# Kernel tuning notes

Hardware: AMD Instinct MI355X
Metric: run time of the kernel (lower is better)

## Reference

```python
import jax, jax.numpy as jnp
import numpy as np

B, S, D = 2, 512, 256      # batch, seq_len, d_model
N = 16                     # d_state
DC = 4                     # d_conv
DI = 2 * D                 # d_inner
CHUNK = 32                 # scan remat chunk size (S % CHUNK == 0)


def setup_inputs() -> dict:
    key = jax.random.key(0)
    ks = jax.random.split(key, 10)
    sc = 0.02
    return {
        "x": jax.random.normal(ks[0], (B, S, D), jnp.float32),
        "adjacency_matrix": jax.random.uniform(ks[1], (B, S, S), dtype=jnp.float32),
        "ln_w": jnp.ones((D,), jnp.float32),
        "ln_b": jnp.zeros((D,), jnp.float32),
        "W_in": jax.random.normal(ks[2], (2 * DI, D), jnp.float32) * sc,
        "conv_w": jax.random.normal(ks[3], (DI, DI, DC), jnp.float32) * sc,
        "conv_b": jnp.zeros((DI,), jnp.float32),
        "W_xp": jax.random.normal(ks[4], (2 * N + 1, DI), jnp.float32) * sc,
        "W_dt": jax.random.normal(ks[5], (DI, 1), jnp.float32) * sc,
        "b_dt": jnp.zeros((DI,), jnp.float32),
        "Wr": jax.random.normal(ks[6], (N, N), jnp.float32) * sc,
        "br": jnp.zeros((N,), jnp.float32),
        "W_out": jax.random.normal(ks[7], (D, DI), jnp.float32) * sc,
    }


def _forward(x, adj, ln_w, ln_b, W_in, conv_w, conv_b, W_xp, W_dt, b_dt, Wr, br, W_out):
    residual = x
    # LayerNorm (biased variance, eps=1e-5, matching nn.LayerNorm)
    mu = x.mean(-1, keepdims=True)
    var = ((x - mu) ** 2).mean(-1, keepdims=True)
    xn = (x - mu) * jax.lax.rsqrt(var + 1e-5) * ln_w + ln_b
    # in_proj (no bias), chunk into x branch and gate z
    xz = xn @ W_in.T                                  # [B,S,2*DI]
    xp, z = xz[..., :DI], xz[..., DI:]
    # causal-ish conv1d with padding d_conv-1, then slice to seq_len
    xc = jax.lax.conv_general_dilated(
        xp.transpose(0, 2, 1), conv_w, (1,), [(DC - 1, DC - 1)],
        dimension_numbers=("NCH", "OIH", "NCH"))
    xc = (xc + conv_b[None, :, None])[..., :S].transpose(0, 2, 1)  # [B,S,DI]
    x_act = jax.nn.silu(xc)
    # x_proj (no bias) -> delta(1), B(N), C(N)
    ssm = x_act @ W_xp.T                              # [B,S,2N+1]
    delta = jax.nn.softplus(ssm[..., :1] @ W_dt.T + b_dt)  # [B,S,DI]
    Bm, Cm = ssm[..., 1:1 + N], ssm[..., 1 + N:]      # [B,S,N]
    pos = jnp.arange(S)

    def step(carry, xs):
        h, hist = xs_carry = carry
        t, d_t, B_t, C_t, x_t, a_t = xs
        # exponential-decay state update: h [B,DI,N]
        h = h * jnp.exp(-d_t)[..., None] + x_t[..., None] * B_t[:, None, :]
        # adjacency-gated, degree-normalized aggregation over prior states
        w = a_t * (pos < t)                           # [B,S], zeros for s>=t
        deg = jnp.maximum(w.sum(-1), 1.0)             # clamp(min=1.0)
        g = jnp.einsum('bs,sbdn->bdn', w, hist) / deg[:, None, None]
        boost = 0.1 * jax.nn.silu(g @ Wr.T + br)
        # torch skips the boost when t==0 or all causal weights are zero
        h = h + jnp.where((t > 0) & jnp.any(w > 0), boost, jnp.zeros_like(boost))
        hist = hist.at[t].set(h)
        y = jnp.einsum('bdn,bn->bd', h, C_t)
        return (h, hist), y

    xs = (pos,
          delta.transpose(1, 0, 2), Bm.transpose(1, 0, 2), Cm.transpose(1, 0, 2),
          x_act.transpose(1, 0, 2), adj.transpose(1, 0, 2))
    nchunks = S // CHUNK
    xs = jax.tree_util.tree_map(lambda a: a.reshape(nchunks, CHUNK, *a.shape[1:]), xs)
    carry0 = (jnp.zeros((B, DI, N), jnp.float32),
              jnp.zeros((S, B, DI, N), jnp.float32))

    @jax.checkpoint
    def chunk_body(carry, xs_c):
        return jax.lax.scan(step, carry, xs_c)

    _, ys = jax.lax.scan(chunk_body, carry0, xs)
    y = ys.reshape(S, B, DI).transpose(1, 0, 2)       # [B,S,DI]
    return (y * jax.nn.silu(z)) @ W_out.T + residual


def reference(x, adjacency_matrix, ln_w, ln_b, W_in, conv_w, conv_b, W_xp, W_dt, b_dt, Wr, br, W_out):
    return _forward(x, adjacency_matrix, ln_w, ln_b, W_in, conv_w, conv_b,
                    W_xp, W_dt, b_dt, Wr, br, W_out)
```

## Files before the change

### kernel.cpp

```cpp
#include <hip/hip_runtime.h>
#include <math.h>

static constexpr int B  = 2;
static constexpr int S  = 512;
static constexpr int D  = 256;
static constexpr int N  = 16;
static constexpr int DI = 512;
static constexpr int CHUNK = 32;
static constexpr int NCHUNK = S / CHUNK;
static constexpr int NL2 = 4;
static constexpr int DN = DI * N;
static constexpr int NSLOT = 8;

typedef unsigned int uint32;
typedef unsigned short ushort16;
using bf16x8 = __attribute__((ext_vector_type(8))) short;
using f32x4  = __attribute__((ext_vector_type(4))) float;

__device__ __forceinline__ ushort16 f2bf(float f) {
    uint32 u = __float_as_uint(f);
    u = (u + 0x7fffu + ((u >> 16) & 1u)) >> 16;
    return (ushort16)u;
}
__device__ __forceinline__ float bflo(uint32 u) { return __uint_as_float(u << 16); }
__device__ __forceinline__ float bfhi(uint32 u) { return __uint_as_float(u & 0xffff0000u); }
__device__ __forceinline__ float bf2f(ushort16 u) { return __uint_as_float(((uint32)u) << 16); }
__device__ __forceinline__ uint32 pk2(float a, float b) {
    return (uint32)(ushort16)f2bf(a) | ((uint32)(ushort16)f2bf(b) << 16);
}
template<int K>
__device__ __forceinline__ float rork(float x) {
    return __uint_as_float((uint32)__builtin_amdgcn_mov_dpp(
        (int)__float_as_uint(x), 0x120 + K, 0xf, 0xf, false));
}
__device__ __forceinline__ size_t htIdx(int b, int dn, int sb) {
    return ((size_t)(b * (S / 32) + sb) * DN + dn) * 32;
}

__global__ void ln_k(const float* __restrict__ x, const float* __restrict__ w,
                     const float* __restrict__ bias, ushort16* __restrict__ xnb) {
    int row = blockIdx.x;
    int lane = threadIdx.x;
    float4 v = *(const float4*)(x + row * D + lane * 4);
    float s = v.x + v.y + v.z + v.w;
    float q = v.x * v.x + v.y * v.y + v.z * v.z + v.w * v.w;
    for (int m = 1; m < 64; m <<= 1) { s += __shfl_xor(s, m); q += __shfl_xor(q, m); }
    float mu  = s * (1.0f / D);
    float var = q * (1.0f / D) - mu * mu;
    float rs  = rsqrtf(var + 1e-5f);
    float4 wv = *(const float4*)(w + lane * 4);
    float4 bv = *(const float4*)(bias + lane * 4);
    float4 o;
    o.x = (v.x - mu) * rs * wv.x + bv.x;
    o.y = (v.y - mu) * rs * wv.y + bv.y;
    o.z = (v.z - mu) * rs * wv.z + bv.z;
    o.w = (v.w - mu) * rs * wv.w + bv.w;
    uint2 pk;
    pk.x = pk2(o.x, o.y);
    pk.y = pk2(o.z, o.w);
    *(uint2*)(xnb + row * D + lane * 4) = pk;
}

template<int MODE>
__global__ __launch_bounds__(256) void gemmb_k(const ushort16* __restrict__ A,
                                               const float* __restrict__ W,
                                               const float* __restrict__ res,
                                               float* __restrict__ C,
                                               ushort16* __restrict__ xpb,
                                               float* __restrict__ zs,
                                               int M, int Nc, int K) {
    __shared__ __align__(16) short As[64 * 40];
    __shared__ __align__(16) short Ws[64 * 40];
    int tid = threadIdx.x;
    int l = tid & 63, wid = tid >> 6;
    int wm = wid & 1, wn = wid >> 1;
    int row0 = blockIdx.y * 64, col0 = blockIdx.x * 64;
    int r = tid >> 2, kseg = (tid & 3) * 8;
    f32x4 acc[2][2] = {};
    for (int k0 = 0; k0 < K; k0 += 32) {
        *(uint4*)&As[r * 40 + kseg] = *(const uint4*)(A + (size_t)(row0 + r) * K + k0 + kseg);
        {
            const float* wrow = W + (size_t)(col0 + r) * K + k0 + kseg;
            float4 w0 = *(const float4*)wrow;
            float4 w1 = *(const float4*)(wrow + 4);
            uint4 q;
            q.x = pk2(w0.x, w0.y); q.y = pk2(w0.z, w0.w);
            q.z = pk2(w1.x, w1.y); q.w = pk2(w1.z, w1.w);
            *(uint4*)&Ws[r * 40 + kseg] = q;
        }
        __syncthreads();
        bf16x8 aF[2], bF[2];
        #pragma unroll
        for (int am = 0; am < 2; ++am)
            aF[am] = *(const bf16x8*)&As[(wm * 32 + am * 16 + (l & 15)) * 40 + (l >> 4) * 8];
        #pragma unroll
        for (int bn = 0; bn < 2; ++bn)
            bF[bn] = *(const bf16x8*)&Ws[(wn * 32 + bn * 16 + (l & 15)) * 40 + (l >> 4) * 8];
        #pragma unroll
        for (int am = 0; am < 2; ++am)
            #pragma unroll
            for (int bn = 0; bn < 2; ++bn)
                acc[am][bn] = __builtin_amdgcn_mfma_f32_16x16x32_bf16(aF[am], bF[bn], acc[am][bn], 0, 0, 0);
        __syncthreads();
    }
    #pragma unroll
    for (int am = 0; am < 2; ++am)
        #pragma unroll
        for (int bn = 0; bn < 2; ++bn) {
            int cc = col0 + wn * 32 + bn * 16 + (l & 15);
            #pragma unroll
            for (int reg = 0; reg < 4; ++reg) {
                int rr = row0 + wm * 32 + am * 16 + (l >> 4) * 4 + reg;
                float v = acc[am][bn][reg];
                if (MODE == 0) {
                    if (res) v += res[(size_t)rr * Nc + cc];
                    C[(size_t)rr * Nc + cc] = v;
                } else {
                    int b = rr >> 9, t = rr & (S - 1);
                    if (cc < DI)
                        xpb[((size_t)(b * (S + 3) + 3 + t)) * DI + cc] = f2bf(v);
                    else
                        zs[((size_t)(b * S + t)) * DI + (cc - DI)] = v / (1.0f + __expf(-v));
                }
            }
        }
}

__global__ __launch_bounds__(256) void convm_k(const ushort16* __restrict__ xpb,
                                               const float* __restrict__ conv_w,
                                               const float* __restrict__ conv_b,
                                               float* __restrict__ x_act) {
    __shared__ __align__(16) short AxS[35 * 40];
    __shared__ __align__(16) short WbS[4 * 32 * 40];
    int tid = threadIdx.x;
    int l = tid & 63, wid = tid >> 6;
    int wm = wid & 1, wn = wid >> 1;
    int o0 = blockIdx.x * 32;
    int mt = blockIdx.y;
    int b = mt >> 4, tl0 = (mt & 15) * 32;
    f32x4 acc = {0.f, 0.f, 0.f, 0.f};

    for (int k0 = 0; k0 < DI; k0 += 32) {
        if (tid < 140) {
            int rr = tid >> 2, seg = tid & 3;
            uint4 v = *(const uint4*)(xpb + ((size_t)(b * (S + 3) + tl0 + rr)) * DI + k0 + seg * 8);
            *(uint4*)&AxS[rr * 40 + seg * 8] = v;
        }
        #pragma unroll
        for (int it = 0; it < 4; ++it) {
            int p = it * 256 + tid;
            int o = p >> 5, i = p & 31;
            float4 w4 = *(const float4*)(conv_w + ((size_t)(o0 + o) * DI + (k0 + i)) * 4);
            WbS[(0 * 32 + o) * 40 + i] = (short)f2bf(w4.x);
            WbS[(1 * 32 + o) * 40 + i] = (short)f2bf(w4.y);
            WbS[(2 * 32 + o) * 40 + i] = (short)f2bf(w4.z);
            WbS[(3 * 32 + o) * 40 + i] = (short)f2bf(w4.w);
        }
        __syncthreads();
        #pragma unroll
        for (int k = 0; k < 4; ++k) {
            bf16x8 aF = *(const bf16x8*)&AxS[(wm * 16 + (l & 15) + k) * 40 + (l >> 4) * 8];
            bf16x8 bF = *(const bf16x8*)&WbS[(k * 32 + wn * 16 + (l & 15)) * 40 + (l >> 4) * 8];
            acc = __builtin_amdgcn_mfma_f32_16x16x32_bf16(aF, bF, acc, 0, 0, 0);
        }
        __syncthreads();
    }
    int oc = o0 + wn * 16 + (l & 15);
    float bia = conv_b[oc];
    #pragma unroll
    for (int reg = 0; reg < 4; ++reg) {
        int m = wm * 16 + (l >> 4) * 4 + reg;
        float v = acc[reg] + bia;
        x_act[((size_t)(b * S + tl0 + m)) * DI + oc] = v / (1.0f + __expf(-v));
    }
}

__global__ void ssmE_k(const float* __restrict__ x_act, const float* __restrict__ W_xp,
                       const float* __restrict__ W_dt, const float* __restrict__ b_dt,
                       float* __restrict__ Bm, float* __restrict__ Cm,
                       float* __restrict__ E) {
    int row = blockIdx.x * 4 + (threadIdx.x >> 6);
    int lane = threadIdx.x & 63;
    const float* xr = x_act + (size_t)row * DI + lane * 8;
    float4 v0 = *(const float4*)xr;
    float4 v1 = *(const float4*)(xr + 4);
    float dtr = 0.0f;
    for (int j = 0; j < 2 * N + 1; ++j) {
        const float* wr = W_xp + (size_t)j * DI + lane * 8;
        float4 w0 = *(const float4*)wr;
        float4 w1 = *(const float4*)(wr + 4);
        float acc = v0.x * w0.x + v0.y * w0.y + v0.z * w0.z + v0.w * w0.w
                  + v1.x * w1.x + v1.y * w1.y + v1.z * w1.z + v1.w * w1.w;
        for (int m = 1; m < 64; m <<= 1) acc += __shfl_xor(acc, m);
        if (j == 0) dtr = acc;
        if (lane == 0) {
            if (j >= 1 && j < 1 + N) Bm[(size_t)row * N + (j - 1)] = acc;
            else if (j >= 1 + N)     Cm[(size_t)row * N + (j - 1 - N)] = acc;
        }
    }
    int d0 = lane * 8;
    float4 w0 = *(const float4*)(W_dt + d0);
    float4 w1 = *(const float4*)(W_dt + d0 + 4);
    float4 q0 = *(const float4*)(b_dt + d0);
    float4 q1 = *(const float4*)(b_dt + d0 + 4);
    float4 e0, e1;
    e0.x = 1.0f / (1.0f + __expf(dtr * w0.x + q0.x));
    e0.y = 1.0f / (1.0f + __expf(dtr * w0.y + q0.y));
    e0.z = 1.0f / (1.0f + __expf(dtr * w0.z + q0.z));
    e0.w = 1.0f / (1.0f + __expf(dtr * w0.w + q0.w));
    e1.x = 1.0f / (1.0f + __expf(dtr * w1.x + q1.x));
    e1.y = 1.0f / (1.0f + __expf(dtr * w1.y + q1.y));
    e1.z = 1.0f / (1.0f + __expf(dtr * w1.z + q1.z));
    e1.w = 1.0f / (1.0f + __expf(dtr * w1.w + q1.w));
    *(float4*)(E + (size_t)row * DI + d0) = e0;
    *(float4*)(E + (size_t)row * DI + d0 + 4) = e1;
}

__global__ void deg_k(const float* __restrict__ adj, float* __restrict__ rdeg, int* __restrict__ flagI) {
    int t = blockIdx.x & (S - 1), b = blockIdx.x >> 9;
    int lane = threadIdx.x;
    const float* row = adj + ((size_t)(b * S + t)) * S;
    float s = 0.0f; bool anyp = false;
    for (int i = lane; i < t; i += 64) { float v = row[i]; s += v; anyp |= (v > 0.0f); }
    for (int m = 1; m < 64; m <<= 1) s += __shfl_xor(s, m);
    bool any = __any(anyp);
    if (lane == 0) {
        rdeg[b * S + t] = 1.0f / fmaxf(s, 1.0f);
        if (t > 0 && any) atomicOr(flagI + t, 1);
    }
}

#define SCAN32(RO, ADJT, GSUM)                                              \
    _Pragma("unroll")                                                       \
    for (int j = 0; j < CHUNK; ++j) {                                       \
        float e  = eL [((RO) + j) * 8 + grp];                               \
        float xa = xaL[((RO) + j) * 8 + grp];                               \
        float Bn = BnL[((RO) + j) * 16 + n];                                \
        h = h * e + xa * Bn;                                                \
        float g0 = GSUM[j], g1 = 0.f, g2 = 0.f, g3 = 0.f;                   \
        const float* ar = (ADJT) + j * 36;                                  \
        int sp = 0;                                                         \
        _Pragma("unroll")                                                   \
        for (; sp + 4 <= j; sp += 4) {                                      \
            float4 av = *(const float4*)(ar + sp);                          \
            g0 += av.x * hreg[sp];     g1 += av.y * hreg[sp + 1];           \
            g2 += av.z * hreg[sp + 2]; g3 += av.w * hreg[sp + 3];           \
        }                                                                   \
        _Pragma("unroll")                                                   \
        for (; sp < j; ++sp) g0 += ar[sp] * hreg[sp];                       \
        float gr = (g0 + g1) + (g2 + g3);                                   \
        float m0 = gr * wrr[0] + rork<4>(gr) * wrr[4]                       \
                 + rork<8>(gr) * wrr[8] + rork<12>(gr) * wrr[12];           \
        float m1 = rork<1>(gr) * wrr[1] + rork<5>(gr) * wrr[5]              \
                 + rork<9>(gr) * wrr[9] + rork<13>(gr) * wrr[13];           \
        float m2 = rork<2>(gr) * wrr[2] + rork<6>(gr) * wrr[6]              \
                 + rork<10>(gr) * wrr[10] + rork<14>(gr) * wrr[14];         \
        float m3 = rork<3>(gr) * wrr[3] + rork<7>(gr) * wrr[7]              \
                 + rork<11>(gr) * wrr[11] + rork<15>(gr) * wrr[15];         \
        float acc = fmaf(rdegL[(RO) + j], (m0 + m1) + (m2 + m3), brn);      \
        if (flL[(RO) + j])                                                  \
            h = fmaf(0.1f * acc,                                            \
                     __builtin_amdgcn_rcpf(1.0f + __expf(-acc)), h);        \
        hreg[j] = h;                                                        \
    }

#define PRESUM(GSUM, PTR) {                                                 \
    const ushort16* _p = (PTR);                                             \
    _Pragma("unroll")                                                       \
    for (int qi = 0; qi < 4; ++qi) {                                        \
        uint4 q = *(const uint4*)(_p + qi * 8);                             \
        GSUM[qi*8+0] += bflo(q.x); GSUM[qi*8+1] += bfhi(q.x);               \
        GSUM[qi*8+2] += bflo(q.y); GSUM[qi*8+3] += bfhi(q.y);               \
        GSUM[qi*8+4] += bflo(q.z); GSUM[qi*8+5] += bfhi(q.z);               \
        GSUM[qi*8+6] += bflo(q.w); GSUM[qi*8+7] += bfhi(q.w);               \
    } }

#define HWRITE(CIDX, HTBUF) {                                               \
    ushort16* ht = histT + htIdx(b, dn, (CIDX));                            \
    _Pragma("unroll")                                                       \
    for (int qi = 0; qi < 4; ++qi) {                                        \
        uint4 q;                                                            \
        q.x = pk2(hreg[qi*8+0], hreg[qi*8+1]);                              \
        q.y = pk2(hreg[qi*8+2], hreg[qi*8+3]);                              \
        q.z = pk2(hreg[qi*8+4], hreg[qi*8+5]);                              \
        q.w = pk2(hreg[qi*8+6], hreg[qi*8+7]);                              \
        *(uint4*)(ht + qi * 8) = q;                                         \
        *(uint4*)&(HTBUF)[qi * 1024 + tid * 8] = q;                         \
    } }

#define MIDPHASE(TCL) {                                                     \
    int w = tid >> 6, l = tid & 63;                                         \
    int ksg = (l >> 4) * 8;                                                 \
    f32x4 ac0[4] = {}, ac1[4] = {};                                         \
    _Pragma("unroll")                                                       \
    for (int sidx = 0; sidx < (TCL); ++sidx) {                              \
        const float* p0 = adj + ((size_t)(b * S + c0s + (TCL) * 32 + (l & 15))) * S \
                        + c0s + sidx * 32 + ksg;                            \
        const float* p1 = p0 + 16 * S;                                      \
        float4 a00 = *(const float4*)p0, a01 = *(const float4*)(p0 + 4);    \
        float4 a10 = *(const float4*)p1, a11 = *(const float4*)(p1 + 4);    \
        uint4 qa, qb;                                                       \
        qa.x = pk2(a00.x, a00.y); qa.y = pk2(a00.z, a00.w);                 \
        qa.z = pk2(a01.x, a01.y); qa.w = pk2(a01.z, a01.w);                 \
        qb.x = pk2(a10.x, a10.y); qb.y = pk2(a10.z, a10.w);                 \
        qb.z = pk2(a11.x, a11.y); qb.w = pk2(a11.z, a11.w);                 \
        bf16x8 aF0, aF1;                                                    \
        *(uint4*)&aF0 = qa; *(uint4*)&aF1 = qb;                             \
        const short* hTs = hTarr[sidx];                                     \
        _Pragma("unroll")                                                   \
        for (int dblk = 0; dblk < 4; ++dblk) {                              \
            int col = w * 64 + dblk * 16 + (l & 15);                        \
            bf16x8 bF = *(const bf16x8*)&hTs[(l >> 4) * 1024 + col * 8];    \
            ac0[dblk] = __builtin_amdgcn_mfma_f32_16x16x32_bf16(aF0, bF, ac0[dblk], 0, 0, 0); \
            ac1[dblk] = __builtin_amdgcn_mfma_f32_16x16x32_bf16(aF1, bF, ac1[dblk], 0, 0, 0); \
        }                                                                   \
    }                                                                       \
    int jb0 = (l >> 4) * 4;                                                 \
    _Pragma("unroll")                                                       \
    for (int dblk = 0; dblk < 4; ++dblk) {                                  \
        int col = w * 64 + dblk * 16 + (l & 15);                            \
        _Pragma("unroll")                                                   \
        for (int reg = 0; reg < 4; ++reg) {                                 \
            Gmid[(jb0 + reg) * 136 + col]      = (short)f2bf(ac0[dblk][reg]); \
            Gmid[(16 + jb0 + reg) * 136 + col] = (short)f2bf(ac1[dblk][reg]); \
        }                                                                   \
    } }

#define GSADD(GSUM)                                                         \
    _Pragma("unroll")                                                       \
    for (int j = 0; j < CHUNK; ++j)                                         \
        GSUM[j] += bf2f((ushort16)Gmid[j * 136 + tid]);

__global__ __launch_bounds__(256) void chunk4_k(const float* __restrict__ adj,
                                                const float* __restrict__ x_act,
                                                const float* __restrict__ E,
                                                const float* __restrict__ Bm,
                                                const float* __restrict__ rdeg,
                                                const int* __restrict__ flagI,
                                                const float* __restrict__ Wr,
                                                const float* __restrict__ br,
                                                ushort16* __restrict__ Gall,
                                                ushort16* __restrict__ histT,
                                                float* __restrict__ hlast, int lc) {
    __shared__ __align__(16) char smem[51200];
    int tid = threadIdx.x;
    int c0 = 4 * lc;
    int c0s = c0 * CHUNK;
    const size_t SLOT = (size_t)B * DN * 32;
    int rp = lc & 1, wp = (lc + 1) & 1;

    if (blockIdx.x < 128) {
        float* triA  = (float*)smem;
        float* triB  = (float*)(smem + 4608);
        float* eL    = (float*)(smem + 9216);
        float* xaL   = (float*)(smem + 11264);
        float* BnL   = (float*)(smem + 13312);
        float* rdegL = (float*)(smem + 17408);
        int*   flL   = (int*)  (smem + 17664);
        short* hTA   = (short*)(smem + 17920);
        short* hTB   = (short*)(smem + 26112);
        short* hTC   = (short*)(smem + 34304);
        short* Gmid  = (short*)(smem + 42496);
        short* hTD   = (short*)(smem + 42496);

        int b = blockIdx.x >> 6;
        int d0 = (blockIdx.x & 63) << 3;
        int n = tid & 15, grp = (tid >> 4) & 7;
        int d = d0 + grp;
        int dn = d * N + n;
        int dnbase = (blockIdx.x & 63) << 7;
        const short* hTarr[4] = {hTA, hTB, hTC, hTD};

        {
            int j = tid >> 3, s4 = (tid & 7) * 4;
            {
                float4 a0 = *(const float4*)(adj + ((size_t)(b * S + c0s + j)) * S + c0s + s4);
                float* dp = triA + j * 36 + s4;
                dp[0] = a0.x; dp[1] = a0.y; dp[2] = a0.z; dp[3] = a0.w;
            }
            {
                float4 a0 = *(const float4*)(adj + ((size_t)(b * S + c0s + 32 + j)) * S + c0s + 32 + s4);
                float* dp = triB + j * 36 + s4;
                dp[0] = a0.x; dp[1] = a0.y; dp[2] = a0.z; dp[3] = a0.w;
            }
            int jr = tid >> 2, dd = (tid & 3) * 2;
            float2 ev = *(const float2*)(E     + ((size_t)(b * S + c0s + jr)) * DI + d0 + dd);
            float2 xv = *(const float2*)(x_act + ((size_t)(b * S + c0s + jr)) * DI + d0 + dd);
            eL [jr * 8 + dd] = ev.x; eL [jr * 8 + dd + 1] = ev.y;
            xaL[jr * 8 + dd] = xv.x; xaL[jr * 8 + dd + 1] = xv.y;
            int nn = (tid & 3) * 4;
            float4 bv = *(const float4*)(Bm + ((size_t)(b * S + c0s + jr)) * N + nn);
            BnL[jr * 16 + nn] = bv.x; BnL[jr * 16 + nn + 1] = bv.y;
            BnL[jr * 16 + nn + 2] = bv.z; BnL[jr * 16 + nn + 3] = bv.w;
            if (tid < 64) {
                rdegL[tid] = rdeg[b * S + c0s + tid];
                flL[tid]   = flagI[c0s + tid];
            }
        }
        __syncthreads();

        float gs0[CHUNK], gs1[CHUNK];
        float wrr[16];
        float brn = 0.f, h = 0.f;
        float hreg[CHUNK];

        if (tid < 128) {
            #pragma unroll
            for (int j = 0; j < CHUNK; ++j) { gs0[j] = 0.f; gs1[j] = 0.f; }
            size_t tb = ((size_t)b * DN + dn) * 32;
            if (lc >= 2) {
                PRESUM(gs0, Gall + ((size_t)rp * NSLOT + 0) * SLOT + tb);
                PRESUM(gs1, Gall + ((size_t)rp * NSLOT + 1) * SLOT + tb);
            }
            if (lc >= 1) {
                PRESUM(gs0, Gall + ((size_t)rp * NSLOT + 4) * SLOT + tb);
                PRESUM(gs1, Gall + ((size_t)rp * NSLOT + 5) * SLOT + tb);
            }
            int probe = __builtin_amdgcn_mov_dpp((int)n, 0x121, 0xf, 0xf, false);
            bool plusdir = (probe == ((n + 1) & 15));
            #pragma unroll
            for (int k = 0; k < 16; ++k) {
                int ip = (n + k) & 15, im = (n - k + 16) & 15;
                wrr[k] = Wr[n * 16 + (plusdir ? ip : im)];
            }
            brn = br[n];
            h = (lc == 0) ? 0.0f : hlast[b * DN + dn];

            SCAN32(0, triA, gs0)
            HWRITE(c0 + 0, hTA)
        }
        __syncthreads();
        if (tid < 128) MIDPHASE(1)
        __syncthreads();
        if (tid < 128) {
            GSADD(gs1)
            SCAN32(32, triB, gs1)
            HWRITE(c0 + 1, hTB)
        }
        __syncthreads();

        {
            int j = tid >> 3, s4 = (tid & 7) * 4;
            {
                float4 a0 = *(const float4*)(adj + ((size_t)(b * S + c0s + 64 + j)) * S + c0s + 64 + s4);
                float* dp = triA + j * 36 + s4;
                dp[0] = a0.x; dp[1] = a0.y; dp[2] = a0.z; dp[3] = a0.w;
            }
            {
                float4 a0 = *(const float4*)(adj + ((size_t)(b * S + c0s + 96 + j)) * S + c0s + 96 + s4);
                float* dp = triB + j * 36 + s4;
                dp[0] = a0.x; dp[1] = a0.y; dp[2] = a0.z; dp[3] = a0.w;
            }
            int jr = tid >> 2, dd = (tid & 3) * 2;
            float2 ev = *(const float2*)(E     + ((size_t)(b * S + c0s + 64 + jr)) * DI + d0 + dd);
            float2 xv = *(const float2*)(x_act + ((size_t)(b * S + c0s + 64 + jr)) * DI + d0 + dd);
            eL [jr * 8 + dd] = ev.x; eL [jr * 8 + dd + 1] = ev.y;
            xaL[jr * 8 + dd] = xv.x; xaL[jr * 8 + dd + 1] = xv.y;
            int nn = (tid & 3) * 4;
            float4 bv = *(const float4*)(Bm + ((size_t)(b * S + c0s + 64 + jr)) * N + nn);
            BnL[jr * 16 + nn] = bv.x; BnL[jr * 16 + nn + 1] = bv.y;
            BnL[jr * 16 + nn + 2] = bv.z; BnL[jr * 16 + nn + 3] = bv.w;
            if (tid < 64) {
                rdegL[tid] = rdeg[b * S + c0s + 64 + tid];
                flL[tid]   = flagI[c0s + 64 + tid];
            }
        }
        if (tid < 128) {
            #pragma unroll
            for (int j = 0; j < CHUNK; ++j) { gs0[j] = 0.f; gs1[j] = 0.f; }
            size_t tb = ((size_t)b * DN + dn) * 32;
            if (lc >= 2) {
                PRESUM(gs0, Gall + ((size_t)rp * NSLOT + 2) * SLOT + tb);
                PRESUM(gs1, Gall + ((size_t)rp * NSLOT + 3) * SLOT + tb);
            }
            if (lc >= 1) {
                PRESUM(gs0, Gall + ((size_t)rp * NSLOT + 6) * SLOT + tb);
                PRESUM(gs1, Gall + ((size_t)rp * NSLOT + 7) * SLOT + tb);
            }
        }
        __syncthreads();
        if (tid < 128) MIDPHASE(2)
        __syncthreads();
        if (tid < 128) {
            GSADD(gs0)
            SCAN32(0, triA, gs0)
            HWRITE(c0 + 2, hTC)
        }
        __syncthreads();
        if (tid < 128) MIDPHASE(3)
        __syncthreads();
        if (tid < 128) GSADD(gs1)
        __syncthreads();
        if (tid < 128) {
            SCAN32(32, triB, gs1)
            HWRITE(c0 + 3, hTD)
            hlast[b * DN + dn] = h;
        }
        __syncthreads();

        if (lc < NL2 - 1) {
            int half = tid >> 7;
            int lt = tid & 127;
            int w = lt >> 6, l = lt & 63;
            int ksg = (l >> 4) * 8;
            int jb0 = (l >> 4) * 4;
            #pragma unroll
            for (int tp = 0; tp < 2; ++tp) {
                int tgt = half * 2 + tp;
                f32x4 ac0[4] = {}, ac1[4] = {};
                #pragma unroll
                for (int src = 0; src < 4; ++src) {
                    const short* hTs = hTarr[src];
                    const float* p0 = adj + ((size_t)(b * S + (4 * (lc + 1) + tgt) * 32 + (l & 15))) * S
                                    + (4 * lc + src) * 32 + ksg;
                    const float* p1 = p0 + 16 * S;
                    float4 a00 = *(const float4*)p0, a01 = *(const float4*)(p0 + 4);
                    float4 a10 = *(const float4*)p1, a11 = *(const float4*)(p1 + 4);
                    uint4 qa, qb;
                    qa.x = pk2(a00.x, a00.y); qa.y = pk2(a00.z, a00.w);
                    qa.z = pk2(a01.x, a01.y); qa.w = pk2(a01.z, a01.w);
                    qb.x = pk2(a10.x, a10.y); qb.y = pk2(a10.z, a10.w);
                    qb.z = pk2(a11.x, a11.y); qb.w = pk2(a11.z, a11.w);
                    bf16x8 aF0, aF1;
                    *(uint4*)&aF0 = qa; *(uint4*)&aF1 = qb;
                    #pragma unroll
                    for (int dblk = 0; dblk < 4; ++dblk) {
                        int col = w * 64 + dblk * 16 + (l & 15);
                        bf16x8 bF = *(const bf16x8*)&hTs[(l >> 4) * 1024 + col * 8];
                        ac0[dblk] = __builtin_amdgcn_mfma_f32_16x16x32_bf16(aF0, bF, ac0[dblk], 0, 0, 0);
                        ac1[dblk] = __builtin_amdgcn_mfma_f32_16x16x32_bf16(aF1, bF, ac1[dblk], 0, 0, 0);
                    }
                }
                ushort16* gw = Gall + ((size_t)wp * NSLOT + (4 + tgt)) * SLOT;
                #pragma unroll
                for (int dblk = 0; dblk < 4; ++dblk) {
                    int col = w * 64 + dblk * 16 + (l & 15);
                    int dng = dnbase + col;
                    uint2 o0, o1;
                    o0.x = pk2(ac0[dblk][0], ac0[dblk][1]); o0.y = pk2(ac0[dblk][2], ac0[dblk][3]);
                    o1.x = pk2(ac1[dblk][0], ac1[dblk][1]); o1.y = pk2(ac1[dblk][2], ac1[dblk][3]);
                    *(uint2*)(gw + ((size_t)b * DN + dng) * 32 + jb0) = o0;
                    *(uint2*)(gw + ((size_t)b * DN + dng) * 32 + 16 + jb0) = o1;
                }
            }
        }
    } else {
        if (lc == 0 || lc >= NL2 - 1) return;
        int idx = blockIdx.x - 128;
        int tile = idx & 63;
        int b = (idx >> 6) & 1;
        int tgt = idx >> 7;
        int tc = 4 * (lc + 1) + tgt;
        int dn0 = tile * 128;
        int w = tid >> 6, l = tid & 63;
        int jh = w & 1, dh = w >> 1;
        int ksg = (l >> 4) * 8;
        const float* abase = adj + ((size_t)(b * S + tc * CHUNK + jh * 16 + (l & 15))) * S + ksg;
        int dnrow = dn0 + dh * 64 + (l & 15);
        int K = 4 * lc;
        f32x4 acc[4] = {};
        #pragma unroll 2
        for (int ks = 0; ks < K; ++ks) {
            float4 af0 = *(const float4*)(abase + ks * 32);
            float4 af1 = *(const float4*)(abase + ks * 32 + 4);
            uint4 aP;
            aP.x = pk2(af0.x, af0.y); aP.y = pk2(af0.z, af0.w);
            aP.z = pk2(af1.x, af1.y); aP.w = pk2(af1.z, af1.w);
            bf16x8 aF;
            *(uint4*)&aF = aP;
            uint4 bP[4];
            #pragma unroll
            for (int dblk = 0; dblk < 4; ++dblk)
                bP[dblk] = *(const uint4*)(histT + htIdx(b, dnrow + dblk * 16, ks) + ksg);
            #pragma unroll
            for (int dblk = 0; dblk < 4; ++dblk) {
                bf16x8 bF;
                *(uint4*)&bF = bP[dblk];
                acc[dblk] = __builtin_amdgcn_mfma_f32_16x16x32_bf16(aF, bF, acc[dblk], 0, 0, 0);
            }
        }
        int jb = jh * 16 + (l >> 4) * 4;
        ushort16* gbase = Gall + ((size_t)wp * NSLOT + tgt) * SLOT;
        #pragma unroll
        for (int dblk = 0; dblk < 4; ++dblk) {
            int dnc = dn0 + dh * 64 + dblk * 16 + (l & 15);
            uint2 o;
            o.x = pk2(acc[dblk][0], acc[dblk][1]);
            o.y = pk2(acc[dblk][2], acc[dblk][3]);
            *(uint2*)(gbase + ((size_t)b * DN + dnc) * 32 + jb) = o;
        }
    }
}

__global__ __launch_bounds__(256) void y_k(const ushort16* __restrict__ histT,
                                           const float* __restrict__ Cm,
                                           const float* __restrict__ zs,
                                           ushort16* __restrict__ yzb) {
    __shared__ float CmL[S * 17];
    int b = blockIdx.x >> 9;
    int d = blockIdx.x & (DI - 1);
    int tid = threadIdx.x;
    #pragma unroll
    for (int q = 0; q < 8; ++q) {
        int l0 = q * 1024 + tid * 4;
        int t = l0 >> 4, n0 = l0 & 15;
        float4 v = *(const float4*)(Cm + (size_t)b * S * N + l0);
        CmL[t * 17 + n0]     = v.x;
        CmL[t * 17 + n0 + 1] = v.y;
        CmL[t * 17 + n0 + 2] = v.z;
        CmL[t * 17 + n0 + 3] = v.w;
    }
    __syncthreads();
    #pragma unroll
    for (int pass = 0; pass < 2; ++pass) {
        int t = pass * 256 + tid;
        int sb = t >> 5, si = t & 31;
        const ushort16* hb = histT + htIdx(b, d * N, sb) + si;
        float a0 = 0.f, a1 = 0.f, a2 = 0.f, a3 = 0.f;
        #pragma unroll
        for (int n = 0; n < 16; n += 4) {
            a0 += bf2f(hb[(size_t)n * 32])       * CmL[t * 17 + n];
            a1 += bf2f(hb[(size_t)(n + 1) * 32]) * CmL[t * 17 + n + 1];
            a2 += bf2f(hb[(size_t)(n + 2) * 32]) * CmL[t * 17 + n + 2];
            a3 += bf2f(hb[(size_t)(n + 3) * 32]) * CmL[t * 17 + n + 3];
        }
        float acc = (a0 + a1) + (a2 + a3);
        float zv = zs[((size_t)(b * S + t)) * DI + d];
        yzb[((size_t)(b * S + t)) * DI + d] = f2bf(acc * zv);
    }
}

extern "C" void kernel_launch(void* const* d_in, const int* in_sizes, int n_in,
                              void* d_out, int out_size, void* d_ws, size_t ws_size,
                              hipStream_t stream) {
    const float* x      = (const float*)d_in[0];
    const float* adj    = (const float*)d_in[1];
    const float* ln_w   = (const float*)d_in[2];
    const float* ln_b   = (const float*)d_in[3];
    const float* W_in   = (const float*)d_in[4];
    const float* conv_w = (const float*)d_in[5];
    const float* conv_b = (const float*)d_in[6];
    const float* W_xp   = (const float*)d_in[7];
    const float* W_dt   = (const float*)d_in[8];
    const float* b_dt   = (const float*)d_in[9];
    const float* Wr     = (const float*)d_in[10];
    const float* br     = (const float*)d_in[11];
    const float* W_out  = (const float*)d_in[12];
    float* out = (float*)d_out;

    float* ws = (float*)d_ws;
    size_t off = 0;
    float* x_act  = ws + off; off += (size_t)B * S * DI;
    float* Bmb    = ws + off; off += (size_t)B * S * N;
    float* Cmb    = ws + off; off += (size_t)B * S * N;
    float* rdegp  = ws + off; off += (size_t)B * S;
    int*   flagI  = (int*)(ws + off); off += S;
    float* Ebuf   = ws + off; off += (size_t)B * S * DI;
    float* zsbuf  = ws + off; off += (size_t)B * S * DI;
    float* hlast  = ws + off; off += (size_t)B * DN;
    ushort16* xnb    = (ushort16*)(ws + off); off += (size_t)B * S * D / 2;
    ushort16* yzb    = (ushort16*)(ws + off); off += (size_t)B * S * DI / 2;
    ushort16* histT  = (ushort16*)(ws + off); off += (size_t)B * DN * S / 2;
    ushort16* Gall   = (ushort16*)(ws + off); off += (size_t)2 * NSLOT * B * DN * 32 / 2;
    ushort16* xpb    = (ushort16*)(ws + off); off += (size_t)B * (S + 3) * DI / 2;

    hipMemsetAsync(flagI, 0, S * sizeof(int), stream);
    hipMemsetAsync(xpb, 0, (size_t)B * (S + 3) * DI * 2, stream);

    ln_k<<<B * S, 64, 0, stream>>>(x, ln_w, ln_b, xnb);
    gemmb_k<1><<<dim3(2 * DI / 64, B * S / 64), 256, 0, stream>>>(
        xnb, W_in, nullptr, nullptr, xpb, zsbuf, B * S, 2 * DI, D);
    convm_k<<<dim3(DI / 32, B * S / 32), 256, 0, stream>>>(xpb, conv_w, conv_b, x_act);
    ssmE_k<<<B * S / 4, 256, 0, stream>>>(x_act, W_xp, W_dt, b_dt, Bmb, Cmb, Ebuf);
    deg_k<<<B * S, 64, 0, stream>>>(adj, rdegp, flagI);

    for (int lc = 0; lc < NL2; ++lc)
        chunk4_k<<<640, 256, 0, stream>>>(adj, x_act, Ebuf, Bmb, rdegp, flagI,
                                          Wr, br, Gall, histT, hlast, lc);

    y_k<<<B * DI, 256, 0, stream>>>(histT, Cmb, zsbuf, yzb);

    gemmb_k<0><<<dim3(D / 64, B * S / 64), 256, 0, stream>>>(
        yzb, W_out, x, out, nullptr, nullptr, B * S, D, DI);
}
```

Baseline: 257.1 us.

## Fuse chunked scan launches into one persistent kernel computing history contributions inline

Replaces four launches of a 640-block chunk kernel with one 128-block kernel that loops over all chunk groups. The cross-group history contributions, previously precomputed by 512 helper blocks into a global Gall buffer, are now computed by the scan blocks themselves with MFMA over all earlier history. The carried state stays in registers, so the hlast buffer and the inter-launch round trips go away. The cost is serialised long-range GEMM work inside only 128 blocks (the K length grows with each group), which loses the parallelism the helper blocks provided.

```diff
diff --git a/kernel.cpp b/kernel.cpp
--- a/kernel.cpp
+++ b/kernel.cpp
@@ -8,9 +8,7 @@
 static constexpr int DI = 512;
 static constexpr int CHUNK = 32;
 static constexpr int NCHUNK = S / CHUNK;
-static constexpr int NL2 = 4;
 static constexpr int DN = DI * N;
-static constexpr int NSLOT = 8;
 
 typedef unsigned int uint32;
 typedef unsigned short ushort16;
@@ -264,17 +262,6 @@
         hreg[j] = h;                                                        \
     }
 
-#define PRESUM(GSUM, PTR) {                                                 \
-    const ushort16* _p = (PTR);                                             \
-    _Pragma("unroll")                                                       \
-    for (int qi = 0; qi < 4; ++qi) {                                        \
-        uint4 q = *(const uint4*)(_p + qi * 8);                             \
-        GSUM[qi*8+0] += bflo(q.x); GSUM[qi*8+1] += bfhi(q.x);               \
-        GSUM[qi*8+2] += bflo(q.y); GSUM[qi*8+3] += bfhi(q.y);               \
-        GSUM[qi*8+4] += bflo(q.z); GSUM[qi*8+5] += bfhi(q.z);               \
-        GSUM[qi*8+6] += bflo(q.w); GSUM[qi*8+7] += bfhi(q.w);               \
-    } }
-
 #define HWRITE(CIDX, HTBUF) {                                               \
     ushort16* ht = histT + htIdx(b, dn, (CIDX));                            \
     _Pragma("unroll")                                                       \
@@ -285,7 +272,7 @@
         q.z = pk2(hreg[qi*8+4], hreg[qi*8+5]);                              \
         q.w = pk2(hreg[qi*8+6], hreg[qi*8+7]);                              \
         *(uint4*)(ht + qi * 8) = q;                                         \
-        *(uint4*)&(HTBUF)[qi * 1024 + tid * 8] = q;                         \
+        if (HTBUF) *(uint4*)&((short*)(HTBUF))[qi * 1024 + tid * 8] = q;    \
     } }
 
 #define MIDPHASE(TCL) {                                                     \
@@ -331,103 +318,148 @@
     for (int j = 0; j < CHUNK; ++j)                                         \
         GSUM[j] += bf2f((ushort16)Gmid[j * 136 + tid]);
 
-__global__ __launch_bounds__(256) void chunk4_k(const float* __restrict__ adj,
-                                                const float* __restrict__ x_act,
-                                                const float* __restrict__ E,
-                                                const float* __restrict__ Bm,
-                                                const float* __restrict__ rdeg,
-                                                const int* __restrict__ flagI,
-                                                const float* __restrict__ Wr,
-                                                const float* __restrict__ br,
-                                                ushort16* __restrict__ Gall,
-                                                ushort16* __restrict__ histT,
-                                                float* __restrict__ hlast, int lc) {
+#define STAGE(OFS) {                                                        \
+    int j = tid >> 3, s4 = (tid & 7) * 4;                                   \
+    {                                                                       \
+        float4 a0 = *(const float4*)(adj + ((size_t)(b * S + c0s + (OFS) + j)) * S + c0s + (OFS) + s4); \
+        float* dp = triA + j * 36 + s4;                                     \
+        dp[0] = a0.x; dp[1] = a0.y; dp[2] = a0.z; dp[3] = a0.w;             \
+    }                                                                       \
+    {                                                                       \
+        float4 a0 = *(const float4*)(adj + ((size_t)(b * S + c0s + (OFS) + 32 + j)) * S + c0s + (OFS) + 32 + s4); \
+        float* dp = triB + j * 36 + s4;                                     \
+        dp[0] = a0.x; dp[1] = a0.y; dp[2] = a0.z; dp[3] = a0.w;             \
+    }                                                                       \
+    int jr = tid >> 2, dd = (tid & 3) * 2;                                  \
+    float2 ev = *(const float2*)(E     + ((size_t)(b * S + c0s + (OFS) + jr)) * DI + d0 + dd); \
+    float2 xv = *(const float2*)(x_act + ((size_t)(b * S + c0s + (OFS) + jr)) * DI + d0 + dd); \
+    eL [jr * 8 + dd] = ev.x; eL [jr * 8 + dd + 1] = ev.y;                   \
+    xaL[jr * 8 + dd] = xv.x; xaL[jr * 8 + dd + 1] = xv.y;                   \
+    int nn = (tid & 3) * 4;                                                 \
+    float4 bv = *(const float4*)(Bm + ((size_t)(b * S + c0s + (OFS) + jr)) * N + nn); \
+    BnL[jr * 16 + nn] = bv.x; BnL[jr * 16 + nn + 1] = bv.y;                 \
+    BnL[jr * 16 + nn + 2] = bv.z; BnL[jr * 16 + nn + 3] = bv.w;             \
+    if (tid < 64) {                                                         \
+        rdegL[tid] = rdeg[b * S + c0s + (OFS) + tid];                       \
+        flL[tid]   = flagI[c0s + (OFS) + tid];                              \
+    } }
+
+#define GOLD2(TCA, TCB, KS1, ACA, ACB) {                                    \
+    int w = tid >> 6, l = tid & 63;                                         \
+    int jh = w >> 1, dh = w & 1;                                            \
+    int ksg = (l >> 4) * 8;                                                 \
+    const float* aA = adj + ((size_t)(b * S + (TCA) * CHUNK + jh * 16 + (l & 15))) * S + ksg; \
+    const float* aB2 = adj + ((size_t)(b * S + (TCB) * CHUNK + jh * 16 + (l & 15))) * S + ksg; \
+    _Pragma("unroll 2")                                                     \
+    for (int ks = 0; ks < (KS1); ++ks) {                                    \
+        uint4 bP[4];                                                        \
+        _Pragma("unroll")                                                   \
+        for (int dblk = 0; dblk < 4; ++dblk)                                \
+            bP[dblk] = *(const uint4*)(histT + htIdx(b, dnbase + dh * 64 + dblk * 16 + (l & 15), ks) + ksg); \
+        float4 fa0 = *(const float4*)(aA + ks * 32);                        \
+        float4 fa1 = *(const float4*)(aA + ks * 32 + 4);                    \
+        float4 fb0 = *(const float4*)(aB2 + ks * 32);                       \
+        float4 fb1 = *(const float4*)(aB2 + ks * 32 + 4);                   \
+        uint4 qa, qb;                                                       \
+        qa.x = pk2(fa0.x, fa0.y); qa.y = pk2(fa0.z, fa0.w);                 \
+        qa.z = pk2(fa1.x, fa1.y); qa.w = pk2(fa1.z, fa1.w);                 \
+        qb.x = pk2(fb0.x, fb0.y); qb.y = pk2(fb0.z, fb0.w);                 \
+        qb.z = pk2(fb1.x, fb1.y); qb.w = pk2(fb1.z, fb1.w);                 \
+        bf16x8 aFA, aFB;                                                    \
+        *(uint4*)&aFA = qa; *(uint4*)&aFB = qb;                             \
+        _Pragma("unroll")                                                   \
+        for (int dblk = 0; dblk < 4; ++dblk) {                              \
+            bf16x8 bF;                                                      \
+            *(uint4*)&bF = bP[dblk];                                        \
+            ACA[dblk] = __builtin_amdgcn_mfma_f32_16x16x32_bf16(aFA, bF, ACA[dblk], 0, 0, 0); \
+            ACB[dblk] = __builtin_amdgcn_mfma_f32_16x16x32_bf16(aFB, bF, ACB[dblk], 0, 0, 0); \
+        }                                                                   \
+    } }
+
+#define GOLDWR(AC) {                                                        \
+    int w = tid >> 6, l = tid & 63;                                         \
+    int jh = w >> 1, dh = w & 1;                                            \
+    int jb0 = jh * 16 + (l >> 4) * 4;                                       \
+    _Pragma("unroll")                                                       \
+    for (int dblk = 0; dblk < 4; ++dblk) {                                  \
+        int col = dh * 64 + dblk * 16 + (l & 15);                           \
+        _Pragma("unroll")                                                   \
+        for (int reg = 0; reg < 4; ++reg)                                   \
+            Gmid[(jb0 + reg) * 136 + col] = (short)f2bf(AC[dblk][reg]);     \
+    } }
+
+__global__ __launch_bounds__(256) void chunkall_k(const float* __restrict__ adj,
+                                                  const float* __restrict__ x_act,
+                                                  const float* __restrict__ E,
+                                                  const float* __restrict__ Bm,
+                                                  const float* __restrict__ rdeg,
+                                                  const int* __restrict__ flagI,
+                                                  const float* __restrict__ Wr,
+                                                  const float* __restrict__ br,
+                                                  ushort16* __restrict__ histT) {
     __shared__ __align__(16) char smem[51200];
+    float* triA  = (float*)smem;
+    float* triB  = (float*)(smem + 4608);
+    float* eL    = (float*)(smem + 9216);
+    float* xaL   = (float*)(smem + 11264);
+    float* BnL   = (float*)(smem + 13312);
+    float* rdegL = (float*)(smem + 17408);
+    int*   flL   = (int*)  (smem + 17664);
+    short* hTA   = (short*)(smem + 17920);
+    short* hTB   = (short*)(smem + 26112);
+    short* hTC   = (short*)(smem + 34304);
+    short* Gmid  = (short*)(smem + 42496);
+
     int tid = threadIdx.x;
-    int c0 = 4 * lc;
-    int c0s = c0 * CHUNK;
-    const size_t SLOT = (size_t)B * DN * 32;
-    int rp = lc & 1, wp = (lc + 1) & 1;
-
-    if (blockIdx.x < 128) {
-        float* triA  = (float*)smem;
-        float* triB  = (float*)(smem + 4608);
-        float* eL    = (float*)(smem + 9216);
-        float* xaL   = (float*)(smem + 11264);
-        float* BnL   = (float*)(smem + 13312);
-        float* rdegL = (float*)(smem + 17408);
-        int*   flL   = (int*)  (smem + 17664);
-        short* hTA   = (short*)(smem + 17920);
-        short* hTB   = (short*)(smem + 26112);
-        short* hTC   = (short*)(smem + 34304);
-        short* Gmid  = (short*)(smem + 42496);
-        short* hTD   = (short*)(smem + 42496);
-
-        int b = blockIdx.x >> 6;
-        int d0 = (blockIdx.x & 63) << 3;
-        int n = tid & 15, grp = (tid >> 4) & 7;
-        int d = d0 + grp;
-        int dn = d * N + n;
-        int dnbase = (blockIdx.x & 63) << 7;
-        const short* hTarr[4] = {hTA, hTB, hTC, hTD};
-
-        {
-            int j = tid >> 3, s4 = (tid & 7) * 4;
-            {
-                float4 a0 = *(const float4*)(adj + ((size_t)(b * S + c0s + j)) * S + c0s + s4);
-                float* dp = triA + j * 36 + s4;
-                dp[0] = a0.x; dp[1] = a0.y; dp[2] = a0.z; dp[3] = a0.w;
-            }
-            {
-                float4 a0 = *(const float4*)(adj + ((size_t)(b * S + c0s + 32 + j)) * S + c0s + 32 + s4);
-                float* dp = triB + j * 36 + s4;
-                dp[0] = a0.x; dp[1] = a0.y; dp[2] = a0.z; dp[3] = a0.w;
-            }
-            int jr = tid >> 2, dd = (tid & 3) * 2;
-            float2 ev = *(const float2*)(E     + ((size_t)(b * S + c0s + jr)) * DI + d0 + dd);
-            float2 xv = *(const float2*)(x_act + ((size_t)(b * S + c0s + jr)) * DI + d0 + dd);
-            eL [jr * 8 + dd] = ev.x; eL [jr * 8 + dd + 1] = ev.y;
-            xaL[jr * 8 + dd] = xv.x; xaL[jr * 8 + dd + 1] = xv.y;
-            int nn = (tid & 3) * 4;
-            float4 bv = *(const float4*)(Bm + ((size_t)(b * S + c0s + jr)) * N + nn);
-            BnL[jr * 16 + nn] = bv.x; BnL[jr * 16 + nn + 1] = bv.y;
-            BnL[jr * 16 + nn + 2] = bv.z; BnL[jr * 16 + nn + 3] = bv.w;
-            if (tid < 64) {
-                rdegL[tid] = rdeg[b * S + c0s + tid];
-                flL[tid]   = flagI[c0s + tid];
-            }
-        }
-        __syncthreads();
-
-        float gs0[CHUNK], gs1[CHUNK];
-        float wrr[16];
-        float brn = 0.f, h = 0.f;
-        float hreg[CHUNK];
-
+    int b = blockIdx.x >> 6;
+    int slice = blockIdx.x & 63;
+    int d0 = slice << 3;
+    int dnbase = slice << 7;
+    int n = tid & 15, grp = (tid >> 4) & 7;
+    int d = d0 + grp;
+    int dn = d * N + n;
+    const short* hTarr[3] = {hTA, hTB, hTC};
+
+    float wrr[16];
+    float brn = 0.f, h = 0.f;
+    float gs0[CHUNK], gs1[CHUNK];
+    float hreg[CHUNK];
+    if (tid < 128) {
+        int probe = __builtin_amdgcn_mov_dpp((int)n, 0x121, 0xf, 0xf, false);
+        bool plusdir = (probe == ((n + 1) & 15));
+        #pragma unroll
+        for (int k = 0; k < 16; ++k) {
+            int ip = (n + k) & 15, im = (n - k + 16) & 15;
+            wrr[k] = Wr[n * 16 + (plusdir ? ip : im)];
+        }
+        brn = br[n];
+    }
+
+    #pragma unroll 1
+    for (int g = 0; g < 4; ++g) {
+        int c0 = 4 * g;
+        int c0s = c0 * CHUNK;
+
+        STAGE(0)
+        __syncthreads();
         if (tid < 128) {
             #pragma unroll
             for (int j = 0; j < CHUNK; ++j) { gs0[j] = 0.f; gs1[j] = 0.f; }
-            size_t tb = ((size_t)b * DN + dn) * 32;
-            if (lc >= 2) {
-                PRESUM(gs0, Gall + ((size_t)rp * NSLOT + 0) * SLOT + tb);
-                PRESUM(gs1, Gall + ((size_t)rp * NSLOT + 1) * SLOT + tb);
-            }
-            if (lc >= 1) {
-                PRESUM(gs0, Gall + ((size_t)rp * NSLOT + 4) * SLOT + tb);
-                PRESUM(gs1, Gall + ((size_t)rp * NSLOT + 5) * SLOT + tb);
-            }
-            int probe = __builtin_amdgcn_mov_dpp((int)n, 0x121, 0xf, 0xf, false);
-            bool plusdir = (probe == ((n + 1) & 15));
-            #pragma unroll
-            for (int k = 0; k < 16; ++k) {
-                int ip = (n + k) & 15, im = (n - k + 16) & 15;
-                wrr[k] = Wr[n * 16 + (plusdir ? ip : im)];
-            }
-            brn = br[n];
-            h = (lc == 0) ? 0.0f : hlast[b * DN + dn];
-
+        }
+        if (g > 0) {
+            f32x4 acA[4] = {}, acB[4] = {};
+            GOLD2(c0, c0 + 1, 4 * g, acA, acB)
+            GOLDWR(acA)
+            __syncthreads();
+            if (tid < 128) GSADD(gs0)
+            __syncthreads();
+            GOLDWR(acB)
+            __syncthreads();
+            if (tid < 128) GSADD(gs1)
+        }
+        if (tid < 128) {
             SCAN32(0, triA, gs0)
-            HWRITE(c0 + 0, hTA)
+            HWRITE(c0, hTA)
         }
         __syncthreads();
         if (tid < 128) MIDPHASE(1)
@@ -439,44 +471,22 @@
         }
         __syncthreads();
 
-        {
-            int j = tid >> 3, s4 = (tid & 7) * 4;
-            {
-                float4 a0 = *(const float4*)(adj + ((size_t)(b * S + c0s + 64 + j)) * S + c0s + 64 + s4);
-                float* dp = triA + j * 36 + s4;
-                dp[0] = a0.x; dp[1] = a0.y; dp[2] = a0.z; dp[3] = a0.w;
-            }
-            {
-                float4 a0 = *(const float4*)(adj + ((size_t)(b * S + c0s + 96 + j)) * S + c0s + 96 + s4);
-                float* dp = triB + j * 36 + s4;
-                dp[0] = a0.x; dp[1] = a0.y; dp[2] = a0.z; dp[3] = a0.w;
-            }
-            int jr = tid >> 2, dd = (tid & 3) * 2;
-            float2 ev = *(const float2*)(E     + ((size_t)(b * S + c0s + 64 + jr)) * DI + d0 + dd);
-            float2 xv = *(const float2*)(x_act + ((size_t)(b * S + c0s + 64 + jr)) * DI + d0 + dd);
-            eL [jr * 8 + dd] = ev.x; eL [jr * 8 + dd + 1] = ev.y;
-            xaL[jr * 8 + dd] = xv.x; xaL[jr * 8 + dd + 1] = xv.y;
-            int nn = (tid & 3) * 4;
-            float4 bv = *(const float4*)(Bm + ((size_t)(b * S + c0s + 64 + jr)) * N + nn);
-            BnL[jr * 16 + nn] = bv.x; BnL[jr * 16 + nn + 1] = bv.y;
-            BnL[jr * 16 + nn + 2] = bv.z; BnL[jr * 16 + nn + 3] = bv.w;
-            if (tid < 64) {
-                rdegL[tid] = rdeg[b * S + c0s + 64 + tid];
-                flL[tid]   = flagI[c0s + 64 + tid];
-            }
-        }
+        STAGE(64)
+        __syncthreads();
         if (tid < 128) {
             #pragma unroll
             for (int j = 0; j < CHUNK; ++j) { gs0[j] = 0.f; gs1[j] = 0.f; }
-            size_t tb = ((size_t)b * DN + dn) * 32;
-            if (lc >= 2) {
-                PRESUM(gs0, Gall + ((size_t)rp * NSLOT + 2) * SLOT + tb);
-                PRESUM(gs1, Gall + ((size_t)rp * NSLOT + 3) * SLOT + tb);
-            }
-            if (lc >= 1) {
-                PRESUM(gs0, Gall + ((size_t)rp * NSLOT + 6) * SLOT + tb);
-                PRESUM(gs1, Gall + ((size_t)rp * NSLOT + 7) * SLOT + tb);
-            }
+        }
+        if (g > 0) {
+            f32x4 acA[4] = {}, acB[4] = {};
+            GOLD2(c0 + 2, c0 + 3, 4 * g, acA, acB)
+            GOLDWR(acA)
+            __syncthreads();
+            if (tid < 128) GSADD(gs0)
+            __syncthreads();
+            GOLDWR(acB)
+            __syncthreads();
+            if (tid < 128) GSADD(gs1)
         }
         __syncthreads();
         if (tid < 128) MIDPHASE(2)
@@ -489,106 +499,12 @@
         __syncthreads();
         if (tid < 128) MIDPHASE(3)
         __syncthreads();
-        if (tid < 128) GSADD(gs1)
-        __syncthreads();
         if (tid < 128) {
+            GSADD(gs1)
             SCAN32(32, triB, gs1)
-            HWRITE(c0 + 3, hTD)
-            hlast[b * DN + dn] = h;
-        }
-        __syncthreads();
-
-        if (lc < NL2 - 1) {
-            int half = tid >> 7;
-            int lt = tid & 127;
-            int w = lt >> 6, l = lt & 63;
-            int ksg = (l >> 4) * 8;
-            int jb0 = (l >> 4) * 4;
-            #pragma unroll
-            for (int tp = 0; tp < 2; ++tp) {
-                int tgt = half * 2 + tp;
-                f32x4 ac0[4] = {}, ac1[4] = {};
-                #pragma unroll
-                for (int src = 0; src < 4; ++src) {
-                    const short* hTs = hTarr[src];
-                    const float* p0 = adj + ((size_t)(b * S + (4 * (lc + 1) + tgt) * 32 + (l & 15))) * S
-                                    + (4 * lc + src) * 32 + ksg;
-                    const float* p1 = p0 + 16 * S;
-                    float4 a00 = *(const float4*)p0, a01 = *(const float4*)(p0 + 4);
-                    float4 a10 = *(const float4*)p1, a11 = *(const float4*)(p1 + 4);
-                    uint4 qa, qb;
-                    qa.x = pk2(a00.x, a00.y); qa.y = pk2(a00.z, a00.w);
-                    qa.z = pk2(a01.x, a01.y); qa.w = pk2(a01.z, a01.w);
-                    qb.x = pk2(a10.x, a10.y); qb.y = pk2(a10.z, a10.w);
-                    qb.z = pk2(a11.x, a11.y); qb.w = pk2(a11.z, a11.w);
-                    bf16x8 aF0, aF1;
-                    *(uint4*)&aF0 = qa; *(uint4*)&aF1 = qb;
-                    #pragma unroll
-                    for (int dblk = 0; dblk < 4; ++dblk) {
-                        int col = w * 64 + dblk * 16 + (l & 15);
-                        bf16x8 bF = *(const bf16x8*)&hTs[(l >> 4) * 1024 + col * 8];
-                        ac0[dblk] = __builtin_amdgcn_mfma_f32_16x16x32_bf16(aF0, bF, ac0[dblk], 0, 0, 0);
-                        ac1[dblk] = __builtin_amdgcn_mfma_f32_16x16x32_bf16(aF1, bF, ac1[dblk], 0, 0, 0);
-                    }
-                }
-                ushort16* gw = Gall + ((size_t)wp * NSLOT + (4 + tgt)) * SLOT;
-                #pragma unroll
-                for (int dblk = 0; dblk < 4; ++dblk) {
-                    int col = w * 64 + dblk * 16 + (l & 15);
-                    int dng = dnbase + col;
-                    uint2 o0, o1;
-                    o0.x = pk2(ac0[dblk][0], ac0[dblk][1]); o0.y = pk2(ac0[dblk][2], ac0[dblk][3]);
-                    o1.x = pk2(ac1[dblk][0], ac1[dblk][1]); o1.y = pk2(ac1[dblk][2], ac1[dblk][3]);
-                    *(uint2*)(gw + ((size_t)b * DN + dng) * 32 + jb0) = o0;
-                    *(uint2*)(gw + ((size_t)b * DN + dng) * 32 + 16 + jb0) = o1;
-                }
-            }
-        }
-    } else {
-        if (lc == 0 || lc >= NL2 - 1) return;
-        int idx = blockIdx.x - 128;
-        int tile = idx & 63;
-        int b = (idx >> 6) & 1;
-        int tgt = idx >> 7;
-        int tc = 4 * (lc + 1) + tgt;
-        int dn0 = tile * 128;
-        int w = tid >> 6, l = tid & 63;
-        int jh = w & 1, dh = w >> 1;
-        int ksg = (l >> 4) * 8;
-        const float* abase = adj + ((size_t)(b * S + tc * CHUNK + jh * 16 + (l & 15))) * S + ksg;
-        int dnrow = dn0 + dh * 64 + (l & 15);
-        int K = 4 * lc;
-        f32x4 acc[4] = {};
-        #pragma unroll 2
-        for (int ks = 0; ks < K; ++ks) {
-            float4 af0 = *(const float4*)(abase + ks * 32);
-            float4 af1 = *(const float4*)(abase + ks * 32 + 4);
-            uint4 aP;
-            aP.x = pk2(af0.x, af0.y); aP.y = pk2(af0.z, af0.w);
-            aP.z = pk2(af1.x, af1.y); aP.w = pk2(af1.z, af1.w);
-            bf16x8 aF;
-            *(uint4*)&aF = aP;
-            uint4 bP[4];
-            #pragma unroll
-            for (int dblk = 0; dblk < 4; ++dblk)
-                bP[dblk] = *(const uint4*)(histT + htIdx(b, dnrow + dblk * 16, ks) + ksg);
-            #pragma unroll
-            for (int dblk = 0; dblk < 4; ++dblk) {
-                bf16x8 bF;
-                *(uint4*)&bF = bP[dblk];
-                acc[dblk] = __builtin_amdgcn_mfma_f32_16x16x32_bf16(aF, bF, acc[dblk], 0, 0, 0);
-            }
-        }
-        int jb = jh * 16 + (l >> 4) * 4;
-        ushort16* gbase = Gall + ((size_t)wp * NSLOT + tgt) * SLOT;
-        #pragma unroll
-        for (int dblk = 0; dblk < 4; ++dblk) {
-            int dnc = dn0 + dh * 64 + dblk * 16 + (l & 15);
-            uint2 o;
-            o.x = pk2(acc[dblk][0], acc[dblk][1]);
-            o.y = pk2(acc[dblk][2], acc[dblk][3]);
-            *(uint2*)(gbase + ((size_t)b * DN + dnc) * 32 + jb) = o;
-        }
+            HWRITE(c0 + 3, (short*)nullptr)
+        }
+        __syncthreads();
     }
 }
 
@@ -657,11 +573,9 @@
     int*   flagI  = (int*)(ws + off); off += S;
     float* Ebuf   = ws + off; off += (size_t)B * S * DI;
     float* zsbuf  = ws + off; off += (size_t)B * S * DI;
-    float* hlast  = ws + off; off += (size_t)B * DN;
     ushort16* xnb    = (ushort16*)(ws + off); off += (size_t)B * S * D / 2;
     ushort16* yzb    = (ushort16*)(ws + off); off += (size_t)B * S * DI / 2;
     ushort16* histT  = (ushort16*)(ws + off); off += (size_t)B * DN * S / 2;
-    ushort16* Gall   = (ushort16*)(ws + off); off += (size_t)2 * NSLOT * B * DN * 32 / 2;
     ushort16* xpb    = (ushort16*)(ws + off); off += (size_t)B * (S + 3) * DI / 2;
 
     hipMemsetAsync(flagI, 0, S * sizeof(int), stream);
@@ -674,9 +588,8 @@
     ssmE_k<<<B * S / 4, 256, 0, stream>>>(x_act, W_xp, W_dt, b_dt, Bmb, Cmb, Ebuf);
     deg_k<<<B * S, 64, 0, stream>>>(adj, rdegp, flagI);
 
-    for (int lc = 0; lc < NL2; ++lc)
-        chunk4_k<<<640, 256, 0, stream>>>(adj, x_act, Ebuf, Bmb, rdegp, flagI,
-                                          Wr, br, Gall, histT, hlast, lc);
+    chunkall_k<<<128, 256, 0, stream>>>(adj, x_act, Ebuf, Bmb, rdegp, flagI,
+                                        Wr, br, histT);
 
     y_k<<<B * DI, 256, 0, stream>>>(histT, Cmb, zsbuf, yzb);
 
```

Measured after the change: 324.7 us. 26.3% more time.

## Compute all four target chunks per block to reuse history loads

Applied to the files above, without the earlier changes.

The off-chunk accumulation blocks now loop over all four target chunks inside one block instead of one target per block. Each histT fragment is loaded once and reused across four MFMA accumulators, and the grid shrinks from 640 to 256 blocks. This cuts redundant history reads, at the cost of more accumulator registers, less parallelism, and a longer serial loop per block.

```diff
diff --git a/kernel.cpp b/kernel.cpp
--- a/kernel.cpp
+++ b/kernel.cpp
@@ -548,46 +548,54 @@
         if (lc == 0 || lc >= NL2 - 1) return;
         int idx = blockIdx.x - 128;
         int tile = idx & 63;
-        int b = (idx >> 6) & 1;
-        int tgt = idx >> 7;
-        int tc = 4 * (lc + 1) + tgt;
+        int b = idx >> 6;
         int dn0 = tile * 128;
         int w = tid >> 6, l = tid & 63;
         int jh = w & 1, dh = w >> 1;
         int ksg = (l >> 4) * 8;
-        const float* abase = adj + ((size_t)(b * S + tc * CHUNK + jh * 16 + (l & 15))) * S + ksg;
         int dnrow = dn0 + dh * 64 + (l & 15);
         int K = 4 * lc;
-        f32x4 acc[4] = {};
-        #pragma unroll 2
+        const float* abase0 = adj + ((size_t)(b * S + (4 * (lc + 1) + 0) * CHUNK + jh * 16 + (l & 15))) * S + ksg;
+        const float* abase1 = abase0 + (size_t)CHUNK * S;
+        const float* abase2 = abase1 + (size_t)CHUNK * S;
+        const float* abase3 = abase2 + (size_t)CHUNK * S;
+        f32x4 acc[4][4] = {};
+        #pragma unroll 1
         for (int ks = 0; ks < K; ++ks) {
-            float4 af0 = *(const float4*)(abase + ks * 32);
-            float4 af1 = *(const float4*)(abase + ks * 32 + 4);
-            uint4 aP;
-            aP.x = pk2(af0.x, af0.y); aP.y = pk2(af0.z, af0.w);
-            aP.z = pk2(af1.x, af1.y); aP.w = pk2(af1.z, af1.w);
-            bf16x8 aF;
-            *(uint4*)&aF = aP;
-            uint4 bP[4];
-            #pragma unroll
-            for (int dblk = 0; dblk < 4; ++dblk)
-                bP[dblk] = *(const uint4*)(histT + htIdx(b, dnrow + dblk * 16, ks) + ksg);
+            bf16x8 bF[4];
             #pragma unroll
             for (int dblk = 0; dblk < 4; ++dblk) {
-                bf16x8 bF;
-                *(uint4*)&bF = bP[dblk];
-                acc[dblk] = __builtin_amdgcn_mfma_f32_16x16x32_bf16(aF, bF, acc[dblk], 0, 0, 0);
+                uint4 bP = *(const uint4*)(histT + htIdx(b, dnrow + dblk * 16, ks) + ksg);
+                *(uint4*)&bF[dblk] = bP;
+            }
+            #pragma unroll
+            for (int tgt = 0; tgt < 4; ++tgt) {
+                const float* ab = (tgt == 0) ? abase0 : (tgt == 1) ? abase1
+                                : (tgt == 2) ? abase2 : abase3;
+                float4 af0 = *(const float4*)(ab + ks * 32);
+                float4 af1 = *(const float4*)(ab + ks * 32 + 4);
+                uint4 aP;
+                aP.x = pk2(af0.x, af0.y); aP.y = pk2(af0.z, af0.w);
+                aP.z = pk2(af1.x, af1.y); aP.w = pk2(af1.z, af1.w);
+                bf16x8 aF;
+                *(uint4*)&aF = aP;
+                #pragma unroll
+                for (int dblk = 0; dblk < 4; ++dblk)
+                    acc[tgt][dblk] = __builtin_amdgcn_mfma_f32_16x16x32_bf16(aF, bF[dblk], acc[tgt][dblk], 0, 0, 0);
             }
         }
         int jb = jh * 16 + (l >> 4) * 4;
-        ushort16* gbase = Gall + ((size_t)wp * NSLOT + tgt) * SLOT;
-        #pragma unroll
-        for (int dblk = 0; dblk < 4; ++dblk) {
-            int dnc = dn0 + dh * 64 + dblk * 16 + (l & 15);
-            uint2 o;
-            o.x = pk2(acc[dblk][0], acc[dblk][1]);
-            o.y = pk2(acc[dblk][2], acc[dblk][3]);
-            *(uint2*)(gbase + ((size_t)b * DN + dnc) * 32 + jb) = o;
+        #pragma unroll
+        for (int tgt = 0; tgt < 4; ++tgt) {
+            ushort16* gbase = Gall + ((size_t)wp * NSLOT + tgt) * SLOT;
+            #pragma unroll
+            for (int dblk = 0; dblk < 4; ++dblk) {
+                int dnc = dn0 + dh * 64 + dblk * 16 + (l & 15);
+                uint2 o;
+                o.x = pk2(acc[tgt][dblk][0], acc[tgt][dblk][1]);
+                o.y = pk2(acc[tgt][dblk][2], acc[tgt][dblk][3]);
+                *(uint2*)(gbase + ((size_t)b * DN + dnc) * 32 + jb) = o;
+            }
         }
     }
 }
@@ -675,7 +683,7 @@
     deg_k<<<B * S, 64, 0, stream>>>(adj, rdegp, flagI);
 
     for (int lc = 0; lc < NL2; ++lc)
-        chunk4_k<<<640, 256, 0, stream>>>(adj, x_act, Ebuf, Bmb, rdegp, flagI,
+        chunk4_k<<<256, 256, 0, stream>>>(adj, x_act, Ebuf, Bmb, rdegp, flagI,
                                           Wr, br, Gall, histT, hlast, lc);
 
     y_k<<<B * DI, 256, 0, stream>>>(histT, Cmb, zsbuf, yzb);
```

Result: no change. 259.2 us (+0.8%).
